# Optimization experiments

Hardware: AMD Instinct MI355X
Metric: run time of the kernel (lower is better)

The kernel has to match this reference:

```python
import jax, jax.numpy as jnp
import numpy as np

NUM_CLS = 80
TOPK = 100
CONF_THRESH = 0.05
NMS_THRESH = 0.5
INPUT_SIZE = (512, 512)  # (H, W)
STRIDES = (8, 16, 32, 64, 128)
BATCH = 64


def make_pixel_location():
    # Faithful to Detector.set_init(): center (x, y, x, y) of each cell, per level.
    H, W = INPUT_SIZE
    locs = []
    for s in STRIDES:
        hs, ws = H // s, W // s
        ys, xs = jnp.meshgrid(jnp.arange(hs, dtype=jnp.float32),
                              jnp.arange(ws, dtype=jnp.float32), indexing='ij')
        x = xs * s + s / 2.0
        y = ys * s + s / 2.0
        locs.append(jnp.stack([x, y, x, y], axis=-1).reshape(-1, 4))
    return jnp.concatenate(locs, axis=0)  # [HW, 4]


def setup_inputs() -> dict:
    key = jax.random.key(0)
    HW = sum((INPUT_SIZE[0] // s) * (INPUT_SIZE[1] // s) for s in STRIDES)  # 5456
    pred_head = jax.random.normal(key, (BATCH, HW, NUM_CLS + 5), dtype=jnp.float32)
    return {"pred_head": pred_head, "pixel_location": make_pixel_location()}


def _per_image(p_cls, p_loc):
    # p_cls: [HW, C] class scores, p_loc: [HW, 4] decoded boxes
    C = NUM_CLS
    # _topk: per-class top-100, then global top-100 over [C*100]
    tk_s, tk_i = jax.lax.top_k(p_cls.T, TOPK)           # [C, TOPK]
    flat_s = tk_s.reshape(-1)                            # [C*TOPK]
    flat_i = tk_i.reshape(-1)
    top_s, top_ind = jax.lax.top_k(flat_s, TOPK)         # [TOPK]
    top_cls = (top_ind // TOPK).astype(jnp.int32)        # class id
    top_hw = flat_i[top_ind]                             # spatial index
    boxes = p_loc[top_hw]                                # [TOPK, 4]
    valid = top_s >= CONF_THRESH

    # Per-class greedy NMS, vectorized over pairs (boxes already sorted desc by score)
    x1, y1, x2, y2 = boxes[:, 0], boxes[:, 1], boxes[:, 2], boxes[:, 3]
    areas = (x2 - x1) * (y2 - y1)
    xx1 = jnp.maximum(x1[:, None], x1[None, :])
    yy1 = jnp.maximum(y1[:, None], y1[None, :])
    xx2 = jnp.minimum(x2[:, None], x2[None, :])
    yy2 = jnp.minimum(y2[:, None], y2[None, :])
    w = jnp.maximum(1e-28, xx2 - xx1)
    h = jnp.maximum(1e-28, yy2 - yy1)
    inter = w * h
    iou = inter / (areas[:, None] + areas[None, :] - inter)
    idx = jnp.arange(TOPK)
    same_cls = top_cls[:, None] == top_cls[None, :]
    later = idx[None, :] > idx[:, None]
    suppress_mat = (iou > NMS_THRESH) & same_cls & later  # [TOPK, TOPK]

    def body(i, keep):
        kept_i = keep[i]
        return keep & ~(kept_i & suppress_mat[i])

    keep = jax.lax.fori_loop(0, TOPK, body, valid)

    # clip_boxes to image bounds, then normalize by scale (W, H, W, H)
    H, W = INPUT_SIZE
    bx = jnp.stack([jnp.clip(boxes[:, 0], 0.0, W - 1),
                    jnp.clip(boxes[:, 1], 0.0, H - 1),
                    jnp.clip(boxes[:, 2], 0.0, W - 1),
                    jnp.clip(boxes[:, 3], 0.0, H - 1)], axis=-1)
    scale = jnp.array([W, H, W, H], dtype=jnp.float32)
    return bx / scale, top_s, top_cls, keep


def reference(pred_head, pixel_location):
    C = NUM_CLS
    cls_pred = jax.nn.sigmoid(pred_head[:, :, :C])                       # [B, HW, C]
    nks_pred = jax.nn.sigmoid(pred_head[:, :, -1:])                      # [B, HW, 1]
    cls_pred = cls_pred ** (2.0 - nks_pred)
    loc_w = jnp.array([-1.0, -1.0, 1.0, 1.0], dtype=pred_head.dtype)
    loc_pred = jnp.exp(pred_head[:, :, C:-1]) * loc_w + pixel_location   # [B, HW, 4]
    # Fixed-size batched outputs: (bboxes [B,100,4], scores [B,100], classes [B,100], keep mask [B,100])
    return jax.vmap(_per_image)(cls_pred, loc_pred)
```

## Files before the change

kernel.cpp:

```cpp
#include <hip/hip_runtime.h>

#define BATCH 64
#define HW    5456
#define NCH   85
#define NCLS  80
#define TOPK  100
#define XTH   1.734f
#define T0    0.85f
#define CAP   16384
#define LCAP  1024
#define SELCAP 1024
#define CNT_STRIDE 32
#define NV4   ((HW * NCH) / 4)

__global__ __launch_bounds__(256) void k_filter(
        const float* __restrict__ pred, float* __restrict__ candS,
        int* __restrict__ candK, int* __restrict__ candCnt) {
    const int b    = blockIdx.y;
    const int tid  = threadIdx.x;
    const int lane = tid & 63;

    __shared__ float lS[LCAP];
    __shared__ int   lK[LCAP];
    __shared__ int   lCnt, gBase;
    if (tid == 0) lCnt = 0;
    __syncthreads();

    const float* predB = pred + (size_t)b * HW * NCH;
    const float4* base = (const float4*)predB;
    const int stride = gridDim.x * 256;
    for (int i = blockIdx.x * 256 + tid; i < NV4; i += stride) {
        float4 v = base[i];
        float cx[4]; int ck[4], chw[4]; int c = 0;
        if ((v.x >= XTH) | (v.y >= XTH) | (v.z >= XTH) | (v.w >= XTH)) {
            int e0 = i * 4;
            #pragma unroll
            for (int j = 0; j < 4; ++j) {
                float x = (j == 0) ? v.x : (j == 1) ? v.y : (j == 2) ? v.z : v.w;
                if (x >= XTH) {
                    int idx = e0 + j;
                    int hw = (int)(__umulhi((unsigned)idx, 0xC0C0C0C1u) >> 6);
                    int ch = idx - hw * 85;
                    if (ch < NCLS) { cx[c] = x; ck[c] = ch * HW + hw; chw[c] = hw; ++c; }
                }
            }
        }
        #pragma unroll
        for (int r = 0; r < 4; ++r) {
            unsigned long long mr = __ballot(c > r);
            if (mr == 0ull) break;
            bool has = (c > r);
            float s = 0.0f;
            if (has) {
                float nks = predB[(size_t)chw[r] * NCH + (NCH - 1)];
                float pw  = 2.0f - 1.0f / (1.0f + expf(-nks));
                s = exp2f(-pw * log2f(1.0f + expf(-cx[r])));
            }
            unsigned long long m = __ballot(has && (s >= T0));
            if (m == 0ull) continue;
            int nn = __popcll(m);
            int leader = __ffsll(m) - 1;
            int bb = 0;
            if (lane == leader) bb = atomicAdd(&lCnt, nn);
            bb = __shfl(bb, leader);
            if (has && (s >= T0)) {
                int pos = bb + __popcll(m & ((1ull << lane) - 1ull));
                if (pos < LCAP) { lS[pos] = s; lK[pos] = ck[r]; }
            }
        }
    }
    __syncthreads();
    int m = lCnt; if (m > LCAP) m = LCAP;
    if (tid == 0) gBase = atomicAdd(candCnt + b * CNT_STRIDE, m);
    __syncthreads();
    int gb = gBase;
    float* cS = candS + (size_t)b * CAP;
    int*   cK = candK + (size_t)b * CAP;
    for (int i = tid; i < m; i += 256) {
        int p = gb + i;
        if (p < CAP) { cS[p] = lS[i]; cK[p] = lK[i]; }
    }
}

__global__ __launch_bounds__(256) void k_select_nms(
        const float* __restrict__ pred, const float* __restrict__ ploc,
        const float* __restrict__ candS, const int* __restrict__ candK,
        const int* __restrict__ candCnt, float* __restrict__ out) {
    const int b = blockIdx.x;
    const int tid = threadIdx.x;
    __shared__ int   hist[256];
    __shared__ float selS[SELCAP];
    __shared__ int   selK[SELCAP];
    __shared__ int   selCnt, cutBin;
    __shared__ float tS[TOPK];
    __shared__ int   tK[TOPK];
    __shared__ float Bx1[TOPK], By1[TOPK], Bx2[TOPK], By2[TOPK], Bar[TOPK];
    __shared__ int   Bcls[TOPK];
    __shared__ unsigned long long supLo[TOPK], supHi[TOPK];
    __shared__ unsigned long long keepLo, keepHi;

    int n = candCnt[b * CNT_STRIDE];
    if (n > CAP) n = CAP;
    const float* cS = candS + (size_t)b * CAP;
    const int*   cK = candK + (size_t)b * CAP;

    hist[tid] = 0;
    if (tid == 0) selCnt = 0;
    __syncthreads();

    const float lo = T0, invw = 256.0f / (1.0f - T0);
    for (int i = tid; i < n; i += 256) {
        int bin = (int)((cS[i] - lo) * invw);
        bin = bin < 0 ? 0 : (bin > 255 ? 255 : bin);
        atomicAdd(&hist[bin], 1);
    }
    __syncthreads();
    if (tid == 0) {
        int acc = 0, B = 0;
        for (int i = 255; i >= 0; --i) {
            acc += hist[i];
            if (acc >= TOPK) { B = i; break; }
        }
        cutBin = B;
    }
    __syncthreads();
    int B = cutBin;
    for (int i = tid; i < n; i += 256) {
        float s = cS[i];
        int bin = (int)((s - lo) * invw);
        bin = bin < 0 ? 0 : (bin > 255 ? 255 : bin);
        if (bin >= B) {
            int p = atomicAdd(&selCnt, 1);
            if (p < SELCAP) { selS[p] = s; selK[p] = cK[i]; }
        }
    }
    if (tid < TOPK) { tS[tid] = -1.0f; tK[tid] = 0; }
    __syncthreads();
    int K = selCnt; if (K > SELCAP) K = SELCAP;
    for (int t = tid; t < K; t += 256) {
        float s = selS[t]; int k = selK[t];
        int r = 0;
        for (int j = 0; j < K; ++j) {
            float sj = selS[j];
            r += (sj > s) || ((sj == s) && (selK[j] < k));
        }
        if (r < TOPK) { tS[r] = s; tK[r] = k; }
    }
    __syncthreads();

    if (tid < TOPK) {
        int k = tK[tid];
        int cls = k / HW;
        int hw  = k - cls * HW;
        const float* pl = pred + ((size_t)b * HW + hw) * NCH + NCLS;
        float e0 = expf(pl[0]), e1 = expf(pl[1]), e2 = expf(pl[2]), e3 = expf(pl[3]);
        const float* pp = ploc + (size_t)hw * 4;
        float x1 = pp[0] - e0, y1 = pp[1] - e1;
        float x2 = pp[2] + e2, y2 = pp[3] + e3;
        Bx1[tid] = x1; By1[tid] = y1; Bx2[tid] = x2; By2[tid] = y2;
        Bar[tid] = (x2 - x1) * (y2 - y1);
        Bcls[tid] = cls;
    }
    __syncthreads();

    if (tid < TOPK) {
        unsigned long long rlo = 0ull, rhi = 0ull;
        float X1 = Bx1[tid], Y1 = By1[tid], X2 = Bx2[tid], Y2 = By2[tid], A = Bar[tid];
        int c = Bcls[tid];
        for (int j = tid + 1; j < TOPK; ++j) {
            if (Bcls[j] != c) continue;
            float xx1 = fmaxf(Bx1[j], X1), yy1 = fmaxf(By1[j], Y1);
            float xx2 = fminf(Bx2[j], X2), yy2 = fminf(By2[j], Y2);
            float w = fmaxf(1e-28f, xx2 - xx1), h = fmaxf(1e-28f, yy2 - yy1);
            float inter = w * h;
            float iou = inter / (Bar[j] + A - inter);
            if (iou > 0.5f) {
                if (j < 64) rlo |= 1ull << j; else rhi |= 1ull << (j - 64);
            }
        }
        supLo[tid] = rlo; supHi[tid] = rhi;
    }
    __syncthreads();
    if (tid == 0) {
        unsigned long long klo = 0ull, khi = 0ull;
        for (int i = 0; i < TOPK; ++i)
            if (tS[i] >= 0.05f) { if (i < 64) klo |= 1ull << i; else khi |= 1ull << (i - 64); }
        for (int i = 0; i < TOPK; ++i) {
            bool ki = (i < 64) ? ((klo >> i) & 1ull) : ((khi >> (i - 64)) & 1ull);
            if (ki) { klo &= ~supLo[i]; khi &= ~supHi[i]; }
        }
        keepLo = klo; keepHi = khi;
    }
    __syncthreads();

    if (tid < TOPK) {
        int r = b * TOPK + tid;
        const float inv = 1.0f / 512.0f;
        float ox1 = fminf(fmaxf(Bx1[tid], 0.0f), 511.0f) * inv;
        float oy1 = fminf(fmaxf(By1[tid], 0.0f), 511.0f) * inv;
        float ox2 = fminf(fmaxf(Bx2[tid], 0.0f), 511.0f) * inv;
        float oy2 = fminf(fmaxf(By2[tid], 0.0f), 511.0f) * inv;
        bool kp = (tid < 64) ? ((keepLo >> tid) & 1ull) : ((keepHi >> (tid - 64)) & 1ull);
        out[(size_t)r * 4 + 0] = ox1;
        out[(size_t)r * 4 + 1] = oy1;
        out[(size_t)r * 4 + 2] = ox2;
        out[(size_t)r * 4 + 3] = oy2;
        out[BATCH * TOPK * 4 + r] = tS[tid];
        out[BATCH * TOPK * 5 + r] = (float)Bcls[tid];
        out[BATCH * TOPK * 6 + r] = kp ? 1.0f : 0.0f;
    }
}

extern "C" void kernel_launch(void* const* d_in, const int* in_sizes, int n_in,
                              void* d_out, int out_size, void* d_ws, size_t ws_size,
                              hipStream_t stream) {
    const float* pred = (const float*)d_in[0];
    const float* ploc = (const float*)d_in[1];
    float* out = (float*)d_out;

    int*   candCnt = (int*)d_ws;
    float* candS   = (float*)((char*)d_ws + 64 * CNT_STRIDE * 4);
    int*   candK   = (int*)((char*)d_ws + 64 * CNT_STRIDE * 4 + (size_t)BATCH * CAP * 4);

    hipMemsetAsync(d_ws, 0, 64 * CNT_STRIDE * 4, stream);

    dim3 g1(32, BATCH);
    k_filter<<<g1, dim3(256), 0, stream>>>(pred, candS, candK, candCnt);
    k_select_nms<<<dim3(BATCH), dim3(256), 0, stream>>>(pred, ploc, candS, candK,
                                                        candCnt, out);
}
```

Before: 249.7 us.

## Defer score computation and split histogram narrowing into separate parallel kernel

```diff
diff --git a/kernel.cpp b/kernel.cpp
--- a/kernel.cpp
+++ b/kernel.cpp
@@ -9,21 +9,29 @@
 #define T0    0.85f
 #define CAP   16384
 #define LCAP  1024
+#define SCAP  1024
 #define SELCAP 1024
 #define CNT_STRIDE 32
 #define NV4   ((HW * NCH) / 4)
+#define HLO   T0
+#define HINV  (256.0f / (1.0f - T0))
 
 __global__ __launch_bounds__(256) void k_filter(
         const float* __restrict__ pred, float* __restrict__ candS,
-        int* __restrict__ candK, int* __restrict__ candCnt) {
+        int* __restrict__ candK, int* __restrict__ candCnt,
+        int* __restrict__ histG) {
     const int b    = blockIdx.y;
     const int tid  = threadIdx.x;
     const int lane = tid & 63;
 
-    __shared__ float lS[LCAP];
+    __shared__ float lX[LCAP];
     __shared__ int   lK[LCAP];
-    __shared__ int   lCnt, gBase;
-    if (tid == 0) lCnt = 0;
+    __shared__ float sS[SCAP];
+    __shared__ int   sK[SCAP];
+    __shared__ int   hist[256];
+    __shared__ int   lCnt, sCnt, gBase;
+    if (tid == 0) { lCnt = 0; sCnt = 0; }
+    hist[tid] = 0;
     __syncthreads();
 
     const float* predB = pred + (size_t)b * HW * NCH;
@@ -31,7 +39,7 @@
     const int stride = gridDim.x * 256;
     for (int i = blockIdx.x * 256 + tid; i < NV4; i += stride) {
         float4 v = base[i];
-        float cx[4]; int ck[4], chw[4]; int c = 0;
+        float cx[4]; int ck[4]; int c = 0;
         if ((v.x >= XTH) | (v.y >= XTH) | (v.z >= XTH) | (v.w >= XTH)) {
             int e0 = i * 4;
             #pragma unroll
@@ -41,57 +49,117 @@
                     int idx = e0 + j;
                     int hw = (int)(__umulhi((unsigned)idx, 0xC0C0C0C1u) >> 6);
                     int ch = idx - hw * 85;
-                    if (ch < NCLS) { cx[c] = x; ck[c] = ch * HW + hw; chw[c] = hw; ++c; }
+                    if (ch < NCLS) { cx[c] = x; ck[c] = ch * HW + hw; ++c; }
                 }
             }
         }
         #pragma unroll
         for (int r = 0; r < 4; ++r) {
-            unsigned long long mr = __ballot(c > r);
-            if (mr == 0ull) break;
-            bool has = (c > r);
-            float s = 0.0f;
-            if (has) {
-                float nks = predB[(size_t)chw[r] * NCH + (NCH - 1)];
-                float pw  = 2.0f - 1.0f / (1.0f + expf(-nks));
-                s = exp2f(-pw * log2f(1.0f + expf(-cx[r])));
-            }
-            unsigned long long m = __ballot(has && (s >= T0));
-            if (m == 0ull) continue;
+            unsigned long long m = __ballot(c > r);
+            if (m == 0ull) break;
             int nn = __popcll(m);
             int leader = __ffsll(m) - 1;
             int bb = 0;
             if (lane == leader) bb = atomicAdd(&lCnt, nn);
             bb = __shfl(bb, leader);
-            if (has && (s >= T0)) {
+            if (c > r) {
                 int pos = bb + __popcll(m & ((1ull << lane) - 1ull));
-                if (pos < LCAP) { lS[pos] = s; lK[pos] = ck[r]; }
+                if (pos < LCAP) { lX[pos] = cx[r]; lK[pos] = ck[r]; }
             }
         }
     }
     __syncthreads();
     int m = lCnt; if (m > LCAP) m = LCAP;
-    if (tid == 0) gBase = atomicAdd(candCnt + b * CNT_STRIDE, m);
+
+    for (int i = tid; i < m; i += 256) {
+        float x = lX[i];
+        int key = lK[i];
+        int hw  = key % HW;
+        float nks = predB[(size_t)hw * NCH + (NCH - 1)];
+        float pw  = 2.0f - 1.0f / (1.0f + expf(-nks));
+        float s   = exp2f(-pw * log2f(1.0f + expf(-x)));
+        unsigned long long mm = __ballot(s >= T0);
+        if (s >= T0) {
+            int leader = __ffsll(mm) - 1;
+            int bb2 = 0;
+            if (lane == leader) bb2 = atomicAdd(&sCnt, __popcll(mm));
+            bb2 = __shfl(bb2, leader);
+            int pos = bb2 + __popcll(mm & ((1ull << lane) - 1ull));
+            if (pos < SCAP) { sS[pos] = s; sK[pos] = key; }
+            int bin = (int)((s - HLO) * HINV);
+            bin = bin < 0 ? 0 : (bin > 255 ? 255 : bin);
+            atomicAdd(&hist[bin], 1);
+        }
+    }
+    __syncthreads();
+    int ms = sCnt; if (ms > SCAP) ms = SCAP;
+    if (tid == 0) gBase = atomicAdd(candCnt + b * CNT_STRIDE, ms);
     __syncthreads();
     int gb = gBase;
     float* cS = candS + (size_t)b * CAP;
     int*   cK = candK + (size_t)b * CAP;
-    for (int i = tid; i < m; i += 256) {
+    for (int i = tid; i < ms; i += 256) {
         int p = gb + i;
-        if (p < CAP) { cS[p] = lS[i]; cK[p] = lK[i]; }
+        if (p < CAP) { cS[p] = sS[i]; cK[p] = sK[i]; }
+    }
+    if (hist[tid] > 0) atomicAdd(histG + b * 256 + tid, hist[tid]);
+}
+
+__global__ __launch_bounds__(256) void k_narrow(
+        const float* __restrict__ candS, const int* __restrict__ candK,
+        const int* __restrict__ candCnt, const int* __restrict__ histG,
+        float* __restrict__ selS, int* __restrict__ selK,
+        int* __restrict__ selCnt) {
+    const int b = blockIdx.y;
+    const int tid = threadIdx.x;
+    const int lane = tid & 63;
+    __shared__ int hl[256];
+    __shared__ int cutBin;
+    hl[tid] = histG[b * 256 + tid];
+    __syncthreads();
+    if (tid == 0) {
+        int acc = 0, B = 0;
+        for (int i = 255; i >= 0; --i) {
+            acc += hl[i];
+            if (acc >= TOPK) { B = i; break; }
+        }
+        cutBin = B;
+    }
+    __syncthreads();
+    const int B = cutBin;
+    int n = candCnt[b * CNT_STRIDE];
+    if (n > CAP) n = CAP;
+    const float* cS = candS + (size_t)b * CAP;
+    const int*   cK = candK + (size_t)b * CAP;
+    float* oS = selS + (size_t)b * SELCAP;
+    int*   oK = selK + (size_t)b * SELCAP;
+    const int stride = gridDim.x * 256;
+    for (int i = blockIdx.x * 256 + tid; i < n; i += stride) {
+        float s = cS[i];
+        int bin = (int)((s - HLO) * HINV);
+        bin = bin < 0 ? 0 : (bin > 255 ? 255 : bin);
+        bool q = (bin >= B);
+        unsigned long long m = __ballot(q);
+        if (m == 0ull) continue;
+        int leader = __ffsll(m) - 1;
+        int bb = 0;
+        if (lane == leader) bb = atomicAdd(selCnt + b * CNT_STRIDE, __popcll(m));
+        bb = __shfl(bb, leader);
+        if (q) {
+            int pos = bb + __popcll(m & ((1ull << lane) - 1ull));
+            if (pos < SELCAP) { oS[pos] = s; oK[pos] = cK[i]; }
+        }
     }
 }
 
 __global__ __launch_bounds__(256) void k_select_nms(
         const float* __restrict__ pred, const float* __restrict__ ploc,
-        const float* __restrict__ candS, const int* __restrict__ candK,
-        const int* __restrict__ candCnt, float* __restrict__ out) {
+        const float* __restrict__ selSg, const int* __restrict__ selKg,
+        const int* __restrict__ selCnt, float* __restrict__ out) {
     const int b = blockIdx.x;
     const int tid = threadIdx.x;
-    __shared__ int   hist[256];
     __shared__ float selS[SELCAP];
     __shared__ int   selK[SELCAP];
-    __shared__ int   selCnt, cutBin;
     __shared__ float tS[TOPK];
     __shared__ int   tK[TOPK];
     __shared__ float Bx1[TOPK], By1[TOPK], Bx2[TOPK], By2[TOPK], Bar[TOPK];
@@ -99,44 +167,15 @@
     __shared__ unsigned long long supLo[TOPK], supHi[TOPK];
     __shared__ unsigned long long keepLo, keepHi;
 
-    int n = candCnt[b * CNT_STRIDE];
-    if (n > CAP) n = CAP;
-    const float* cS = candS + (size_t)b * CAP;
-    const int*   cK = candK + (size_t)b * CAP;
-
-    hist[tid] = 0;
-    if (tid == 0) selCnt = 0;
-    __syncthreads();
-
-    const float lo = T0, invw = 256.0f / (1.0f - T0);
-    for (int i = tid; i < n; i += 256) {
-        int bin = (int)((cS[i] - lo) * invw);
-        bin = bin < 0 ? 0 : (bin > 255 ? 255 : bin);
-        atomicAdd(&hist[bin], 1);
-    }
-    __syncthreads();
-    if (tid == 0) {
-        int acc = 0, B = 0;
-        for (int i = 255; i >= 0; --i) {
-            acc += hist[i];
-            if (acc >= TOPK) { B = i; break; }
-        }
-        cutBin = B;
-    }
-    __syncthreads();
-    int B = cutBin;
-    for (int i = tid; i < n; i += 256) {
-        float s = cS[i];
-        int bin = (int)((s - lo) * invw);
-        bin = bin < 0 ? 0 : (bin > 255 ? 255 : bin);
-        if (bin >= B) {
-            int p = atomicAdd(&selCnt, 1);
-            if (p < SELCAP) { selS[p] = s; selK[p] = cK[i]; }
-        }
+    int K = selCnt[b * CNT_STRIDE];
+    if (K > SELCAP) K = SELCAP;
+    for (int i = tid; i < K; i += 256) {
+        selS[i] = selSg[(size_t)b * SELCAP + i];
+        selK[i] = selKg[(size_t)b * SELCAP + i];
     }
     if (tid < TOPK) { tS[tid] = -1.0f; tK[tid] = 0; }
     __syncthreads();
-    int K = selCnt; if (K > SELCAP) K = SELCAP;
+
     for (int t = tid; t < K; t += 256) {
         float s = selS[t]; int k = selK[t];
         int r = 0;
@@ -218,14 +257,22 @@
     const float* ploc = (const float*)d_in[1];
     float* out = (float*)d_out;
 
-    int*   candCnt = (int*)d_ws;
-    float* candS   = (float*)((char*)d_ws + 64 * CNT_STRIDE * 4);
-    int*   candK   = (int*)((char*)d_ws + 64 * CNT_STRIDE * 4 + (size_t)BATCH * CAP * 4);
-
-    hipMemsetAsync(d_ws, 0, 64 * CNT_STRIDE * 4, stream);
+    char* w = (char*)d_ws;
+    int*   candCnt = (int*)(w);
+    int*   selCnt  = (int*)(w + 8192);
+    int*   histG   = (int*)(w + 16384);
+    float* candS   = (float*)(w + 81920);
+    int*   candK   = (int*)(w + 81920 + (size_t)BATCH * CAP * 4);
+    float* selS    = (float*)(w + 81920 + (size_t)BATCH * CAP * 8);
+    int*   selK    = (int*)(w + 81920 + (size_t)BATCH * CAP * 8 + BATCH * SELCAP * 4);
+
+    hipMemsetAsync(d_ws, 0, 81920, stream);
 
     dim3 g1(32, BATCH);
-    k_filter<<<g1, dim3(256), 0, stream>>>(pred, candS, candK, candCnt);
-    k_select_nms<<<dim3(BATCH), dim3(256), 0, stream>>>(pred, ploc, candS, candK,
-                                                        candCnt, out);
-}
+    k_filter<<<g1, dim3(256), 0, stream>>>(pred, candS, candK, candCnt, histG);
+    dim3 g2(8, BATCH);
+    k_narrow<<<g2, dim3(256), 0, stream>>>(candS, candK, candCnt, histG,
+                                           selS, selK, selCnt);
+    k_select_nms<<<dim3(BATCH), dim3(256), 0, stream>>>(pred, ploc, selS, selK,
+                                                        selCnt, out);
+}
```

Measured after the change: 225.0 us. -9.9%, faster.
